# Kernel tuning notes

Hardware: AMD Instinct MI355X
Metric: run time of the kernel (lower is better)

## Reference

```python
import jax, jax.numpy as jnp
import numpy as np

NIN = 1024
NOUT = 1024
NHEADS = 16
DHEAD = NOUT // NHEADS


def setup_inputs() -> dict:
    key = jax.random.key(0)
    k1, k2, k3, k4 = jax.random.split(key, 4)
    y = jax.random.normal(k1, (2, 2048, NIN), dtype=jnp.float32)
    Wqkv = jax.random.normal(k2, (NIN, 3 * NOUT), dtype=jnp.float32) * (1.0 / np.sqrt(NIN))
    Wff = jax.random.normal(k3, (NOUT, NOUT), dtype=jnp.float32) * (1.0 / np.sqrt(NOUT))
    bff = jax.random.normal(k4, (NOUT,), dtype=jnp.float32) * 0.01
    return {"y": y, "Wqkv": Wqkv, "Wff": Wff, "bff": bff}


def reference(y, Wqkv, Wff, bff):
    b, n, _ = y.shape
    qkv = y @ Wqkv  # [b, n, 3*nout]
    qkv = qkv.reshape(b, n, 3, NHEADS, DHEAD).transpose(2, 0, 3, 1, 4)
    q, k, v = qkv[0], qkv[1], qkv[2]  # each [b, h, n, d]
    att = jnp.einsum('bhqd,bhkd->bhqk', q, k)
    causal = jnp.triu(jnp.ones((n, n), dtype=bool), k=1)
    att = jnp.where(causal, -jnp.inf, att)
    att = jax.nn.softmax(att / jnp.sqrt(jnp.float32(DHEAD)), axis=-1)
    ctx = jnp.einsum('bhqk,bhkd->bhqd', att, v)
    ctx = ctx.transpose(0, 2, 1, 3).reshape(b, n, NOUT)
    return ctx @ Wff + bff
```

## Files before the change

### kernel.cpp

```cpp
#include <hip/hip_runtime.h>
#include <stdint.h>

#define NHEADS 16
#define DHEAD 64
#define SEQ 2048
#define BATCH 2
#define NINF 1024
#define NOUTF 1024
#define N3 3072
#define MTOT 4096

typedef unsigned short US;
typedef __attribute__((ext_vector_type(8))) short short8;
typedef __attribute__((ext_vector_type(4))) short short4v;
typedef __attribute__((ext_vector_type(4))) float f32x4;

__device__ inline US f2bf(float f) {
  union { float f; unsigned u; } v; v.f = f;
  unsigned r = v.u + 0x7fffu + ((v.u >> 16) & 1u);
  return (US)(r >> 16);
}

__device__ inline f32x4 mfma16(short8 a, short8 b, f32x4 c) {
  return __builtin_amdgcn_mfma_f32_16x16x32_bf16(a, b, c, 0, 0, 0);
}

__device__ inline f32x4 mfma16k16(short4v a, short4v b, f32x4 c) {
  return __builtin_amdgcn_mfma_f32_16x16x16bf16_1k(a, b, c, 0, 0, 0);
}

__device__ inline void async16(const US* g, US* l) {
  __builtin_amdgcn_global_load_lds(
      (const __attribute__((address_space(1))) unsigned int*)g,
      (__attribute__((address_space(3))) unsigned int*)l, 16, 0, 0);
}

__global__ void k_convert(const float* __restrict__ src, US* __restrict__ dst, int n4) {
  int i = blockIdx.x * blockDim.x + threadIdx.x;
  if (i >= n4) return;
  float4 v = ((const float4*)src)[i];
  ushort4 o;
  o.x = f2bf(v.x); o.y = f2bf(v.y); o.z = f2bf(v.z); o.w = f2bf(v.w);
  ((ushort4*)dst)[i] = o;
}

__global__ void k_transpose(const float* __restrict__ src, US* __restrict__ dst,
                            int R, int C) {
  __shared__ float tile[32][33];
  int bx = blockIdx.x * 32, by = blockIdx.y * 32;
  int tx = threadIdx.x, ty = threadIdx.y;
  for (int i = 0; i < 32; i += 8)
    tile[ty + i][tx] = src[(size_t)(by + ty + i) * C + bx + tx];
  __syncthreads();
  for (int i = 0; i < 32; i += 8)
    dst[(size_t)(bx + ty + i) * R + by + tx] = f2bf(tile[tx][ty + i]);
}

__global__ void k_vtrans(const US* __restrict__ src, US* __restrict__ dst) {
  __shared__ US tile[32][33];
  int bh = blockIdx.z;
  int bx = blockIdx.x * 32;
  int by = blockIdx.y * 32;
  int tx = threadIdx.x, ty = threadIdx.y;
  const US* s0 = src + (size_t)bh * SEQ * DHEAD;
  US* d0 = dst + (size_t)bh * DHEAD * SEQ;
  for (int i = 0; i < 32; i += 8)
    tile[ty + i][tx] = s0[(size_t)(by + ty + i) * DHEAD + bx + tx];
  __syncthreads();
  for (int i = 0; i < 32; i += 8)
    d0[(size_t)(bx + ty + i) * SEQ + by + tx] = tile[tx][ty + i];
}

__global__ __launch_bounds__(256) void k_gemm_qkv(
    const US* __restrict__ A,
    const US* __restrict__ Bt,
    US* __restrict__ qbuf, US* __restrict__ kbuf, US* __restrict__ vbuf) {
  __shared__ US As[128 * 32];
  __shared__ US Bs[128 * 32];
  int tid = threadIdx.x;
  int wave = tid >> 6, lane = tid & 63, lm = lane & 15, lk = lane >> 4;
  int wm = wave >> 1, wn = wave & 1;
  int mbase = blockIdx.y * 128, nbase = blockIdx.x * 128;

  f32x4 acc[4][4];
#pragma unroll
  for (int i = 0; i < 4; ++i)
#pragma unroll
    for (int j = 0; j < 4; ++j) acc[i][j] = (f32x4){0.f, 0.f, 0.f, 0.f};

  const US* ga = A + (size_t)(mbase + (tid >> 2)) * NINF + (tid & 3) * 8;
  const US* gb = Bt + (size_t)(nbase + (tid >> 2)) * NINF + (tid & 3) * 8;
  US* la = As + tid * 8;
  US* lb = Bs + tid * 8;

  for (int kt = 0; kt < NINF / 32; ++kt) {
    int ko = kt * 32;
    async16(ga + ko, la);
    async16(ga + ko + (size_t)64 * NINF, la + 64 * 32);
    async16(gb + ko, lb);
    async16(gb + ko + (size_t)64 * NINF, lb + 64 * 32);
    __syncthreads();
    short8 a[4], b[4];
#pragma unroll
    for (int i = 0; i < 4; ++i)
      a[i] = *(const short8*)(As + (wm * 64 + i * 16 + lm) * 32 + lk * 8);
#pragma unroll
    for (int j = 0; j < 4; ++j)
      b[j] = *(const short8*)(Bs + (wn * 64 + j * 16 + lm) * 32 + lk * 8);
#pragma unroll
    for (int i = 0; i < 4; ++i)
#pragma unroll
      for (int j = 0; j < 4; ++j) acc[i][j] = mfma16(a[i], b[j], acc[i][j]);
    __syncthreads();
  }

  int which = nbase >> 10;
  US* dsts = (which == 0) ? qbuf : (which == 1) ? kbuf : vbuf;
#pragma unroll
  for (int j = 0; j < 4; ++j) {
    int col = nbase + wn * 64 + j * 16 + lm;
    int hh = (col & 1023) >> 6;
    int d = col & 63;
#pragma unroll
    for (int i = 0; i < 4; ++i) {
#pragma unroll
      for (int r = 0; r < 4; ++r) {
        int row = mbase + wm * 64 + i * 16 + lk * 4 + r;
        int bb = row >> 11;
        int s = row & (SEQ - 1);
        int bh = bb * NHEADS + hh;
        dsts[((size_t)bh * SEQ + s) * DHEAD + d] = f2bf(acc[i][j][r]);
      }
    }
  }
}

__global__ __launch_bounds__(256) void k_attn(
    const US* __restrict__ qbuf, const US* __restrict__ kbuf,
    const US* __restrict__ vtbuf, US* __restrict__ ctx) {
  __shared__ US Ks[64 * 64];
  __shared__ US Vs[64 * 64];
  int tid = threadIdx.x;
  int w = tid >> 6, lane = tid & 63;
  int lm = lane & 15, lk = lane >> 4;
  int bl = blockIdx.x;
  int xcd = bl & 7, g = bl >> 3;
  int bh = (g & 3) * 8 + xcd;
  int s = 31 - (g >> 2);
  int qb = s * 64 + w * 16;
  int nt = s + 1;
  const float cscale = 0.18033688011112042f;

  const US* kbase = kbuf + (size_t)bh * SEQ * DHEAD;
  const US* vtb = vtbuf + (size_t)bh * DHEAD * SEQ;
  const US* qr = qbuf + ((size_t)bh * SEQ + qb + lm) * DHEAD + lk * 8;
  short8 qf0 = *(const short8*)(qr);
  short8 qf1 = *(const short8*)(qr + 32);

  int swz = ((lane & 7) ^ (lane >> 3)) * 8;
  const US* gsrc[4];
  US* ldst[4];
  int step[4];
#pragma unroll
  for (int j = 0; j < 4; ++j) {
    int u = w + 4 * j;
    if (u < 8) {
      gsrc[j] = kbase + (size_t)(u * 8 + (lane >> 3)) * DHEAD + swz;
      ldst[j] = Ks + u * 512 + lane * 8;
      step[j] = 64 * DHEAD;
    } else {
      int i = u - 8;
      gsrc[j] = vtb + (size_t)(i * 8 + (lane >> 3)) * SEQ + swz;
      ldst[j] = Vs + i * 512 + lane * 8;
      step[j] = 64;
    }
  }

  int xorv = lm & 7;
  int ck0 = ((lk) ^ xorv) * 16;
  int ck1 = ((4 + lk) ^ xorv) * 16;
  int cv[4];
#pragma unroll
  for (int kg = 0; kg < 4; ++kg)
    cv[kg] = (((kg * 2 + (lk >> 1)) ^ xorv) * 16) + (lk & 1) * 8;

  f32x4 o[4];
#pragma unroll
  for (int dg = 0; dg < 4; ++dg) o[dg] = (f32x4){0.f, 0.f, 0.f, 0.f};
  float rsum = 0.f;

  const char* Kc = (const char*)Ks;
  const char* Vc = (const char*)Vs;

  for (int t = 0; t < nt; ++t) {
    __syncthreads();
#pragma unroll
    for (int j = 0; j < 4; ++j) async16(gsrc[j], ldst[j]);
#pragma unroll
    for (int j = 0; j < 4; ++j) gsrc[j] += step[j];
    __syncthreads();

    bool dtile = (t == nt - 1);
    int kgn = dtile ? (w + 1) : 4;
    for (int kg = 0; kg < kgn; ++kg) {
      const char* kr = Kc + (kg * 16 + lm) * 128;
      short8 ka0 = *(const short8*)(kr + ck0);
      short8 ka1 = *(const short8*)(kr + ck1);
      f32x4 st = (f32x4){0.f, 0.f, 0.f, 0.f};
      st = mfma16(ka0, qf0, st);
      st = mfma16(ka1, qf1, st);
      bool dm = dtile && (kg == w);
      float e[4];
#pragma unroll
      for (int r = 0; r < 4; ++r) {
        float v = st[r] * cscale;
        if (dm && (lk * 4 + r > lm)) v = -INFINITY;
        e[r] = exp2f(v);
        rsum += e[r];
      }
      union { short4v s4; uint32_t u[2]; } pk;
      pk.u[0] = (uint32_t)f2bf(e[0]) | ((uint32_t)f2bf(e[1]) << 16);
      pk.u[1] = (uint32_t)f2bf(e[2]) | ((uint32_t)f2bf(e[3]) << 16);
      const char* vr = Vc + lm * 128 + cv[kg];
#pragma unroll
      for (int dg = 0; dg < 4; ++dg) {
        short4v va = *(const short4v*)(vr + dg * 2048);
        o[dg] = mfma16k16(va, pk.s4, o[dg]);
      }
    }
  }

  rsum += __shfl_xor(rsum, 16);
  rsum += __shfl_xor(rsum, 32);
  float inv = 1.f / rsum;

  US* crow = ctx + ((size_t)(bh >> 4) * SEQ + qb + lm) * NOUTF + (bh & 15) * DHEAD;
#pragma unroll
  for (int dg = 0; dg < 4; ++dg) {
    union { short4v s4; uint32_t u[2]; } pk;
    pk.u[0] = (uint32_t)f2bf(o[dg][0] * inv) | ((uint32_t)f2bf(o[dg][1] * inv) << 16);
    pk.u[1] = (uint32_t)f2bf(o[dg][2] * inv) | ((uint32_t)f2bf(o[dg][3] * inv) << 16);
    *(short4v*)(crow + dg * 16 + lk * 4) = pk.s4;
  }
}

__global__ __launch_bounds__(256) void k_gemm_out(
    const US* __restrict__ A, const US* __restrict__ Bt,
    const float* __restrict__ bias, float* __restrict__ out) {
  __shared__ US As[128 * 32];
  __shared__ US Bs[64 * 32];
  int tid = threadIdx.x;
  int wave = tid >> 6, lane = tid & 63, lm = lane & 15, lk = lane >> 4;
  int mbase = blockIdx.y * 128, nbase = blockIdx.x * 64;

  f32x4 acc[2][4];
#pragma unroll
  for (int i = 0; i < 2; ++i)
#pragma unroll
    for (int j = 0; j < 4; ++j) acc[i][j] = (f32x4){0.f, 0.f, 0.f, 0.f};

  const US* ga = A + (size_t)(mbase + (tid >> 2)) * NOUTF + (tid & 3) * 8;
  const US* gb = Bt + (size_t)(nbase + (tid >> 2)) * NOUTF + (tid & 3) * 8;
  US* la = As + tid * 8;
  US* lb = Bs + tid * 8;

  for (int kt = 0; kt < NOUTF / 32; ++kt) {
    int ko = kt * 32;
    async16(ga + ko, la);
    async16(ga + ko + (size_t)64 * NOUTF, la + 64 * 32);
    async16(gb + ko, lb);
    __syncthreads();
    short8 a[2], b[4];
#pragma unroll
    for (int i = 0; i < 2; ++i)
      a[i] = *(const short8*)(As + (wave * 32 + i * 16 + lm) * 32 + lk * 8);
#pragma unroll
    for (int j = 0; j < 4; ++j)
      b[j] = *(const short8*)(Bs + (j * 16 + lm) * 32 + lk * 8);
#pragma unroll
    for (int i = 0; i < 2; ++i)
#pragma unroll
      for (int j = 0; j < 4; ++j) acc[i][j] = mfma16(a[i], b[j], acc[i][j]);
    __syncthreads();
  }

#pragma unroll
  for (int j = 0; j < 4; ++j) {
    int col = nbase + j * 16 + lm;
    float bv = bias[col];
#pragma unroll
    for (int i = 0; i < 2; ++i)
#pragma unroll
      for (int r = 0; r < 4; ++r) {
        int row = mbase + wave * 32 + i * 16 + lk * 4 + r;
        out[(size_t)row * NOUTF + col] = acc[i][j][r] + bv;
      }
  }
}

extern "C" void kernel_launch(void* const* d_in, const int* in_sizes, int n_in,
                              void* d_out, int out_size, void* d_ws, size_t ws_size,
                              hipStream_t stream) {
  const float* y    = (const float*)d_in[0];
  const float* Wqkv = (const float*)d_in[1];
  const float* Wff  = (const float*)d_in[2];
  const float* bff  = (const float*)d_in[3];
  float* out = (float*)d_out;

  char* ws = (char*)d_ws;
  US* ybf   = (US*)(ws);
  US* ctx   = (US*)(ws);
  US* wqkvt = (US*)(ws + (8u << 20));
  US* wfft  = (US*)(ws + (14u << 20));
  US* qbuf  = (US*)(ws + (16u << 20));
  US* kbuf  = (US*)(ws + (24u << 20));
  US* vbuf  = (US*)(ws + (32u << 20));
  US* vtbuf = (US*)(ws + (40u << 20));

  k_convert<<<MTOT * NINF / 4 / 256, 256, 0, stream>>>(y, ybf, MTOT * NINF / 4);
  k_transpose<<<dim3(N3 / 32, NINF / 32), dim3(32, 8), 0, stream>>>(Wqkv, wqkvt, NINF, N3);
  k_transpose<<<dim3(NOUTF / 32, NOUTF / 32), dim3(32, 8), 0, stream>>>(Wff, wfft, NOUTF, NOUTF);
  k_gemm_qkv<<<dim3(N3 / 128, MTOT / 128), 256, 0, stream>>>(ybf, wqkvt, qbuf, kbuf, vbuf);
  k_vtrans<<<dim3(DHEAD / 32, SEQ / 32, BATCH * NHEADS), dim3(32, 8), 0, stream>>>(vbuf, vtbuf);
  k_attn<<<dim3(1024), 256, 0, stream>>>(qbuf, kbuf, vtbuf, ctx);
  k_gemm_out<<<dim3(NOUTF / 64, MTOT / 128), 256, 0, stream>>>(ctx, wfft, bff, out);
}
```

Before: 197.0 us.

## Fold softmax scale into Q projection, sum rows via MFMA, merge weight transposes

The softmax scale multiply moves from the attention inner loop into the QKV GEMM epilogue for Q. The per-lane exp-sum plus shuffles is replaced by an MFMA against a ones vector that accumulates row sums. The bf16 packing now uses add-and-perm (round-half-up instead of round-to-nearest-even), and the last diagonal tile is peeled out of the main loop with full unrolling. The two weight-transpose launches are merged into one kernel. Rounding Q after scaling and the cheaper bf16 rounding change numerics slightly.

```diff
diff --git a/kernel.cpp b/kernel.cpp
--- a/kernel.cpp
+++ b/kernel.cpp
@@ -44,16 +44,20 @@
   ((ushort4*)dst)[i] = o;
 }
 
-__global__ void k_transpose(const float* __restrict__ src, US* __restrict__ dst,
-                            int R, int C) {
+__global__ void k_wtrans(const float* __restrict__ Wqkv, const float* __restrict__ Wff,
+                         US* __restrict__ dq, US* __restrict__ df) {
   __shared__ float tile[32][33];
-  int bx = blockIdx.x * 32, by = blockIdx.y * 32;
+  int bxi = blockIdx.x;
+  const float* src; US* dst; int C;
+  if (bxi < 96) { src = Wqkv; dst = dq; C = N3; }
+  else          { src = Wff;  dst = df; C = NOUTF; bxi -= 96; }
+  int bx = bxi * 32, by = blockIdx.y * 32;
   int tx = threadIdx.x, ty = threadIdx.y;
   for (int i = 0; i < 32; i += 8)
     tile[ty + i][tx] = src[(size_t)(by + ty + i) * C + bx + tx];
   __syncthreads();
   for (int i = 0; i < 32; i += 8)
-    dst[(size_t)(bx + ty + i) * R + by + tx] = f2bf(tile[tx][ty + i]);
+    dst[(size_t)(bx + ty + i) * 1024 + by + tx] = f2bf(tile[tx][ty + i]);
 }
 
 __global__ void k_vtrans(const US* __restrict__ src, US* __restrict__ dst) {
@@ -116,6 +120,7 @@
 
   int which = nbase >> 10;
   US* dsts = (which == 0) ? qbuf : (which == 1) ? kbuf : vbuf;
+  float sc = (which == 0) ? 0.18033688011112042f : 1.f;
 #pragma unroll
   for (int j = 0; j < 4; ++j) {
     int col = nbase + wn * 64 + j * 16 + lm;
@@ -129,7 +134,7 @@
         int bb = row >> 11;
         int s = row & (SEQ - 1);
         int bh = bb * NHEADS + hh;
-        dsts[((size_t)bh * SEQ + s) * DHEAD + d] = f2bf(acc[i][j][r]);
+        dsts[((size_t)bh * SEQ + s) * DHEAD + d] = f2bf(acc[i][j][r] * sc);
       }
     }
   }
@@ -149,7 +154,6 @@
   int s = 31 - (g >> 2);
   int qb = s * 64 + w * 16;
   int nt = s + 1;
-  const float cscale = 0.18033688011112042f;
 
   const US* kbase = kbuf + (size_t)bh * SEQ * DHEAD;
   const US* vtb = vtbuf + (size_t)bh * DHEAD * SEQ;
@@ -187,52 +191,58 @@
   f32x4 o[4];
 #pragma unroll
   for (int dg = 0; dg < 4; ++dg) o[dg] = (f32x4){0.f, 0.f, 0.f, 0.f};
-  float rsum = 0.f;
+  f32x4 lacc = (f32x4){0.f, 0.f, 0.f, 0.f};
+  const short4v kones = {(short)0x3F80, (short)0x3F80, (short)0x3F80, (short)0x3F80};
 
   const char* Kc = (const char*)Ks;
   const char* Vc = (const char*)Vs;
 
-  for (int t = 0; t < nt; ++t) {
+  auto body = [&](int kg, bool dm) {
+    const char* kr = Kc + (kg * 16 + lm) * 128;
+    short8 ka0 = *(const short8*)(kr + ck0);
+    short8 ka1 = *(const short8*)(kr + ck1);
+    f32x4 st = (f32x4){0.f, 0.f, 0.f, 0.f};
+    st = mfma16(ka0, qf0, st);
+    st = mfma16(ka1, qf1, st);
+    uint32_t ue[4];
+#pragma unroll
+    for (int r = 0; r < 4; ++r) {
+      float v = st[r];
+      if (dm && (lk * 4 + r > lm)) v = -INFINITY;
+      union { float f; uint32_t u; } cv2;
+      cv2.f = exp2f(v);
+      ue[r] = cv2.u + 0x8000u;
+    }
+    union { short4v s4; uint32_t u[2]; } pk;
+    pk.u[0] = __builtin_amdgcn_perm(ue[1], ue[0], 0x07060302u);
+    pk.u[1] = __builtin_amdgcn_perm(ue[3], ue[2], 0x07060302u);
+    lacc = mfma16k16(kones, pk.s4, lacc);
+    const char* vr = Vc + lm * 128 + cv[kg];
+#pragma unroll
+    for (int dg = 0; dg < 4; ++dg) {
+      short4v va = *(const short4v*)(vr + dg * 2048);
+      o[dg] = mfma16k16(va, pk.s4, o[dg]);
+    }
+  };
+
+  for (int t = 0; t < nt - 1; ++t) {
     __syncthreads();
 #pragma unroll
     for (int j = 0; j < 4; ++j) async16(gsrc[j], ldst[j]);
 #pragma unroll
     for (int j = 0; j < 4; ++j) gsrc[j] += step[j];
     __syncthreads();
-
-    bool dtile = (t == nt - 1);
-    int kgn = dtile ? (w + 1) : 4;
-    for (int kg = 0; kg < kgn; ++kg) {
-      const char* kr = Kc + (kg * 16 + lm) * 128;
-      short8 ka0 = *(const short8*)(kr + ck0);
-      short8 ka1 = *(const short8*)(kr + ck1);
-      f32x4 st = (f32x4){0.f, 0.f, 0.f, 0.f};
-      st = mfma16(ka0, qf0, st);
-      st = mfma16(ka1, qf1, st);
-      bool dm = dtile && (kg == w);
-      float e[4];
-#pragma unroll
-      for (int r = 0; r < 4; ++r) {
-        float v = st[r] * cscale;
-        if (dm && (lk * 4 + r > lm)) v = -INFINITY;
-        e[r] = exp2f(v);
-        rsum += e[r];
-      }
-      union { short4v s4; uint32_t u[2]; } pk;
-      pk.u[0] = (uint32_t)f2bf(e[0]) | ((uint32_t)f2bf(e[1]) << 16);
-      pk.u[1] = (uint32_t)f2bf(e[2]) | ((uint32_t)f2bf(e[3]) << 16);
-      const char* vr = Vc + lm * 128 + cv[kg];
-#pragma unroll
-      for (int dg = 0; dg < 4; ++dg) {
-        short4v va = *(const short4v*)(vr + dg * 2048);
-        o[dg] = mfma16k16(va, pk.s4, o[dg]);
-      }
-    }
-  }
-
-  rsum += __shfl_xor(rsum, 16);
-  rsum += __shfl_xor(rsum, 32);
-  float inv = 1.f / rsum;
+#pragma unroll
+    for (int kg = 0; kg < 4; ++kg) body(kg, false);
+  }
+  __syncthreads();
+#pragma unroll
+  for (int j = 0; j < 4; ++j) async16(gsrc[j], ldst[j]);
+  __syncthreads();
+  for (int kg = 0; kg < w; ++kg) body(kg, false);
+  body(w, true);
+
+  float inv = 1.f / lacc[0];
 
   US* crow = ctx + ((size_t)(bh >> 4) * SEQ + qb + lm) * NOUTF + (bh & 15) * DHEAD;
 #pragma unroll
@@ -318,8 +328,7 @@
   US* vtbuf = (US*)(ws + (40u << 20));
 
   k_convert<<<MTOT * NINF / 4 / 256, 256, 0, stream>>>(y, ybf, MTOT * NINF / 4);
-  k_transpose<<<dim3(N3 / 32, NINF / 32), dim3(32, 8), 0, stream>>>(Wqkv, wqkvt, NINF, N3);
-  k_transpose<<<dim3(NOUTF / 32, NOUTF / 32), dim3(32, 8), 0, stream>>>(Wff, wfft, NOUTF, NOUTF);
+  k_wtrans<<<dim3(128, 32), dim3(32, 8), 0, stream>>>(Wqkv, Wff, wqkvt, wfft);
   k_gemm_qkv<<<dim3(N3 / 128, MTOT / 128), 256, 0, stream>>>(ybf, wqkvt, qbuf, kbuf, vbuf);
   k_vtrans<<<dim3(DHEAD / 32, SEQ / 32, BATCH * NHEADS), dim3(32, 8), 0, stream>>>(vbuf, vtbuf);
   k_attn<<<dim3(1024), 256, 0, stream>>>(qbuf, kbuf, vtbuf, ctx);
```

After: 191.7 us. -2.7%, faster.
